# Kernel tuning notes

Measured on AMD Instinct MI355X. Metric: run time of the kernel, lower is better.

Reference implementation:

```python
import jax, jax.numpy as jnp
import numpy as np

B, S, D = 2, 2048, 2048
NH, NKV = 16, 4
HD = D // NH          # 128
Q_DIM = NH * HD       # 2048
KV_DIM = NKV * HD     # 512
N_REP = NH // NKV     # 4


def setup_inputs() -> dict:
    key = jax.random.key(0)
    k1, k2, k3, k4 = jax.random.split(key, 4)
    x = jax.random.normal(k1, (B, S, D), dtype=jnp.float32)
    freqs_cis = jax.random.normal(k2, (S, HD), dtype=jnp.float32)
    Wqkv = jax.random.normal(k3, (Q_DIM + 2 * KV_DIM, D), dtype=jnp.float32) * (D ** -0.5)
    Wo = jax.random.normal(k4, (D, Q_DIM), dtype=jnp.float32) * (Q_DIM ** -0.5)
    return {"x": x, "freqs_cis": freqs_cis, "Wqkv": Wqkv, "Wo": Wo}


def _apply_rope(xq, xk, freqs_cis):
    # xq: [B,S,NH,HD], xk: [B,S,NKV,HD], freqs_cis: [S,HD] viewed as [S,1,HD//2,2]
    f = freqs_cis.reshape(S, 1, HD // 2, 2)
    f0, f1 = f[..., 0], f[..., 1]  # broadcast over batch & heads

    def rot(t):
        shp = t.shape
        tp = t.reshape(*shp[:-1], HD // 2, 2)
        t0, t1 = tp[..., 0], tp[..., 1]
        # row1 = <x, (f0,f1)>;  row0 = <x, (f1,-f0)>  (matches torch flip+negate)
        row1 = t0 * f0 + t1 * f1
        row0 = t0 * f1 - t1 * f0
        return jnp.stack([row0, row1], axis=-1).reshape(shp)

    return rot(xq), rot(xk)


def reference(x, freqs_cis, Wqkv, Wo):
    # Fused QKV projection (exact path: all RLA sketch dims = 0)
    xqkv = jnp.einsum('bsd,od->bso', x, Wqkv)
    xq = xqkv[..., :Q_DIM].reshape(B, S, NH, HD)
    xk = xqkv[..., Q_DIM:Q_DIM + KV_DIM].reshape(B, S, NKV, HD)
    xv = xqkv[..., Q_DIM + KV_DIM:].reshape(B, S, NKV, HD)

    xq, xk = _apply_rope(xq, xk, freqs_cis)

    # [B,H,S,HD]
    xq = xq.transpose(0, 2, 1, 3)
    xk = xk.transpose(0, 2, 1, 3)
    xv = xv.transpose(0, 2, 1, 3)

    # GQA: repeat kv heads n_rep times
    xk = jnp.repeat(xk, N_REP, axis=1)
    xv = jnp.repeat(xv, N_REP, axis=1)

    scale = 1.0 / jnp.sqrt(jnp.asarray(HD, dtype=xq.dtype))
    scores = jnp.einsum('bhqd,bhkd->bhqk', xq, xk) * scale
    causal = jnp.tril(jnp.ones((S, S), dtype=bool))
    scores = jnp.where(causal, scores, jnp.finfo(scores.dtype).min)
    probs = jax.nn.softmax(scores, axis=-1)
    out = jnp.einsum('bhqk,bhkd->bhqd', probs, xv)  # [B,H,S,HD]

    out = out.transpose(0, 2, 1, 3).reshape(B, S, Q_DIM)
    return jnp.einsum('bsq,dq->bsd', out, Wo)
```

## Files before the change

### kernel.cpp

```cpp
#include <hip/hip_runtime.h>
#include <hip/hip_bf16.h>
#include <cstdint>
#include <cstddef>

#define B_ 2
#define S_ 2048
#define NH_ 16
#define NKV_ 4
#define HD_ 128
#define QDIM_ 2048
#define KVDIM_ 512
#define QKV_ 3072

typedef __attribute__((ext_vector_type(8))) short short8;
typedef __attribute__((ext_vector_type(4))) short bhalf4;
typedef __attribute__((ext_vector_type(4))) float float4v;

__device__ __forceinline__ float bf2f(short u) {
  union { unsigned int i; float f; } v;
  v.i = ((unsigned int)(unsigned short)u) << 16;
  return v.f;
}
__device__ __forceinline__ short f2bf(float f) {
  union { float f; unsigned int i; } v; v.f = f;
  unsigned int x = v.i;
  x += 0x7fffu + ((x >> 16) & 1u);
  return (short)(x >> 16);
}

__device__ __forceinline__ void async_copy16(void* lds, const void* g) {
  __builtin_amdgcn_global_load_lds(
      (const __attribute__((address_space(1))) void*)g,
      (__attribute__((address_space(3))) void*)lds, 16, 0, 0);
}

__global__ void f32_to_bf16(const float* __restrict__ src, short* __restrict__ dst,
                            int n8) {
  int id = blockIdx.x * 256 + threadIdx.x;
  if (id >= n8) return;
  const float* f = src + (size_t)id * 8;
  float4v a = *(const float4v*)(f);
  float4v b = *(const float4v*)(f + 4);
  short8 r;
#pragma unroll
  for (int e = 0; e < 4; ++e) { r[e] = f2bf(a[e]); r[4 + e] = f2bf(b[e]); }
  *(short8*)(dst + (size_t)id * 8) = r;
}

template <int N, int K, bool CF32>
__global__ __launch_bounds__(256)
void gemm_nt_bf16(const short* __restrict__ A, const short* __restrict__ Bm,
                  void* __restrict__ Cp) {
  __shared__ __align__(16) short sA[128 * 32];
  __shared__ __align__(16) short sB[128 * 32];
  const int tid = threadIdx.x;
  const int m0 = blockIdx.y * 128, n0 = blockIdx.x * 128;
  const int wave = tid >> 6, lane = tid & 63;
  const int wm = (wave & 1) << 6, wn = (wave >> 1) << 6;
  const int lm = lane & 15, kg = lane >> 4;

  float4v acc[4][4];
#pragma unroll
  for (int i = 0; i < 4; ++i)
#pragma unroll
    for (int j = 0; j < 4; ++j)
      acc[i][j] = (float4v){0.f, 0.f, 0.f, 0.f};

  const int r0 = tid >> 2, c0 = tid & 3;
  const short* gA0 = A + (size_t)(m0 + r0) * K + c0 * 8;
  const short* gA1 = gA0 + (size_t)64 * K;
  const short* gB0 = Bm + (size_t)(n0 + r0) * K + c0 * 8;
  const short* gB1 = gB0 + (size_t)64 * K;
  short* lA0 = sA + tid * 8;
  short* lA1 = sA + 2048 + tid * 8;
  short* lB0 = sB + tid * 8;
  short* lB1 = sB + 2048 + tid * 8;

  for (int k0 = 0; k0 < K; k0 += 32) {
    async_copy16(lA0, gA0 + k0);
    async_copy16(lA1, gA1 + k0);
    async_copy16(lB0, gB0 + k0);
    async_copy16(lB1, gB1 + k0);
    __syncthreads();

    short8 a[4], b[4];
#pragma unroll
    for (int i = 0; i < 4; ++i)
      a[i] = *(const short8*)(sA + (wm + i * 16 + lm) * 32 + kg * 8);
#pragma unroll
    for (int j = 0; j < 4; ++j)
      b[j] = *(const short8*)(sB + (wn + j * 16 + lm) * 32 + kg * 8);
#pragma unroll
    for (int i = 0; i < 4; ++i)
#pragma unroll
      for (int j = 0; j < 4; ++j)
        acc[i][j] = __builtin_amdgcn_mfma_f32_16x16x32_bf16(a[i], b[j], acc[i][j], 0, 0, 0);
    __syncthreads();
  }

#pragma unroll
  for (int i = 0; i < 4; ++i) {
    const int rb = m0 + wm + i * 16 + kg * 4;
#pragma unroll
    for (int j = 0; j < 4; ++j) {
      const int cc = n0 + wn + j * 16 + lm;
#pragma unroll
      for (int r = 0; r < 4; ++r) {
        if constexpr (CF32)
          ((float*)Cp)[(size_t)(rb + r) * N + cc] = acc[i][j][r];
        else
          ((short*)Cp)[(size_t)(rb + r) * N + cc] = f2bf(acc[i][j][r]);
      }
    }
  }
}

__global__ void rope_split(const short* __restrict__ xqkv, const float* __restrict__ freqs,
                           short* __restrict__ Qr, short* __restrict__ Kr,
                           short* __restrict__ Vv) {
  const int id = blockIdx.x * 256 + threadIdx.x;
  const int i = id / (QKV_ / 8);
  const int c8 = id % (QKV_ / 8);
  const int col = c8 * 8;
  const int b = i >> 11, s = i & (S_ - 1);
  short8 xv = *(const short8*)(xqkv + (size_t)i * QKV_ + col);
  if (col < QDIM_ + KVDIM_) {
    int d;
    short* dst;
    float sc;
    if (col < QDIM_) {
      int hh = col >> 7; d = col & 127;
      dst = Qr + ((size_t)(b * NH_ + hh) * S_ + s) * HD_ + d;
      sc = 0.08838834764831845f;
    } else {
      int cc = col - QDIM_;
      int hh = cc >> 7; d = cc & 127;
      dst = Kr + ((size_t)(b * NKV_ + hh) * S_ + s) * HD_ + d;
      sc = 1.0f;
    }
    const float* fp = freqs + (size_t)s * HD_ + d;
    float4v fa = *(const float4v*)(fp);
    float4v fb = *(const float4v*)(fp + 4);
    float ff[8] = {fa[0], fa[1], fa[2], fa[3], fb[0], fb[1], fb[2], fb[3]};
    short8 ov;
#pragma unroll
    for (int pp = 0; pp < 4; ++pp) {
      float t0 = bf2f(xv[2 * pp]), t1 = bf2f(xv[2 * pp + 1]);
      float f0 = ff[2 * pp], f1 = ff[2 * pp + 1];
      ov[2 * pp]     = f2bf((t0 * f1 - t1 * f0) * sc);
      ov[2 * pp + 1] = f2bf((t0 * f0 + t1 * f1) * sc);
    }
    *(short8*)dst = ov;
  } else {
    int cc = col - QDIM_ - KVDIM_;
    int hh = cc >> 7, d = cc & 127;
    *(short8*)(Vv + ((size_t)(b * NKV_ + hh) * S_ + s) * HD_ + d) = xv;
  }
}

__global__ void transpose_v(const short* __restrict__ Vv, short* __restrict__ Vt) {
  __shared__ short t[64][72];
  const int s0 = blockIdx.x * 64, d0 = blockIdx.y * 64;
  const short* src = Vv + (size_t)blockIdx.z * S_ * HD_;
  short* dst = Vt + (size_t)blockIdx.z * S_ * HD_;
  const int tid = threadIdx.x;
#pragma unroll
  for (int c = 0; c < 2; ++c) {
    int ch = tid + 256 * c;
    int row = ch >> 3, kc = ch & 7;
    *(short8*)(&t[row][kc * 8]) =
        *(const short8*)(src + (size_t)(s0 + row) * HD_ + d0 + kc * 8);
  }
  __syncthreads();
#pragma unroll
  for (int c = 0; c < 2; ++c) {
    int ch = tid + 256 * c;
    int drow = ch >> 3, sc = ch & 7;
    short8 w;
#pragma unroll
    for (int j = 0; j < 8; ++j) w[j] = t[sc * 8 + j][drow];
    *(short8*)(dst + (size_t)(d0 + drow) * S_ + s0 + sc * 8) = w;
  }
}

#define TK 64

__global__ __launch_bounds__(256)
void attn_causal(const short* __restrict__ Q, const short* __restrict__ K,
                 const short* __restrict__ Vt, short* __restrict__ O) {
  const int pair = blockIdx.x;
  const int bh = blockIdx.y;
  const int b = bh >> 4, h = bh & 15;
  const int kvh = h >> 2;
  const int tid = threadIdx.x, wave = tid >> 6, lane = tid & 63;
  const int lm = lane & 15, kg = lane >> 4;

  __shared__ __align__(16) short sK[TK * HD_];
  __shared__ __align__(16) short sVt[HD_ * TK];
  __shared__ __align__(16) short sO[4 * 16 * 128];

  const short* Qb = Q + (size_t)(b * NH_ + h) * S_ * HD_;
  const short* Kb = K + (size_t)(b * NKV_ + kvh) * S_ * HD_;
  const short* Vtb = Vt + (size_t)(b * NKV_ + kvh) * S_ * HD_;

  for (int half = 0; half < 2; ++half) {
    const int qt = (half == 0) ? pair : 31 - pair;
    const int q0w = qt * 64 + wave * 16;
    const int qglob = q0w + lm;

    short8 qf[4];
#pragma unroll
    for (int kk = 0; kk < 4; ++kk)
      qf[kk] = *(const short8*)(Qb + (size_t)qglob * HD_ + kk * 32 + kg * 8);

    float mcur = -1e9f, lcur = 0.f;
    float4v o[8];
#pragma unroll
    for (int df = 0; df < 8; ++df) o[df] = (float4v){0.f, 0.f, 0.f, 0.f};

    const int ntiles = qt + 1;
    for (int j = 0; j < ntiles; ++j) {
      const int k0 = j * TK;
#pragma unroll
      for (int c = 0; c < 4; ++c) {
        int ch = tid + 256 * c;
        int row = ch >> 4, kc = ch & 15;
        async_copy16(sK + ch * 8,
                     Kb + (size_t)(k0 + row) * HD_ + (kc ^ (row & 7)) * 8);
      }
#pragma unroll
      for (int c = 0; c < 4; ++c) {
        int ch = tid + 256 * c;
        int row = ch >> 3, kc = ch & 7;
        async_copy16(sVt + ch * 8,
                     Vtb + (size_t)row * S_ + k0 + (kc ^ (row & 7)) * 8);
      }
      __syncthreads();

      float4v sfT[4];
#pragma unroll
      for (int mj = 0; mj < 4; ++mj) sfT[mj] = (float4v){0.f, 0.f, 0.f, 0.f};
#pragma unroll
      for (int kk = 0; kk < 4; ++kk) {
        int kd = kk * 4 + kg;
#pragma unroll
        for (int mj = 0; mj < 4; ++mj) {
          int row = mj * 16 + lm;
          short8 af = *(const short8*)(sK + row * HD_ + (kd ^ (row & 7)) * 8);
          sfT[mj] = __builtin_amdgcn_mfma_f32_16x16x32_bf16(af, qf[kk], sfT[mj], 0, 0, 0);
        }
      }

      if (j == qt) {
#pragma unroll
        for (int mj = 0; mj < 4; ++mj)
#pragma unroll
          for (int r = 0; r < 4; ++r) {
            int kcol = k0 + mj * 16 + kg * 4 + r;
            sfT[mj][r] = (kcol <= qglob) ? sfT[mj][r] : -3e38f;
          }
      }

      float mx = -3e38f;
#pragma unroll
      for (int mj = 0; mj < 4; ++mj)
#pragma unroll
        for (int r = 0; r < 4; ++r) mx = fmaxf(mx, sfT[mj][r]);
      mx = fmaxf(mx, __shfl_xor(mx, 16, 64));
      mx = fmaxf(mx, __shfl_xor(mx, 32, 64));
      float mnew = fmaxf(mcur, mx);
      float alpha = __expf(fminf(mcur - mnew, 0.f));
      float rs = 0.f;
      bhalf4 pb[4];
#pragma unroll
      for (int t = 0; t < 4; ++t)
#pragma unroll
        for (int r = 0; r < 4; ++r) {
          float e = __expf(fminf(sfT[t][r] - mnew, 0.f));
          rs += e;
          pb[t][r] = f2bf(e);
        }
      rs += __shfl_xor(rs, 16, 64);
      rs += __shfl_xor(rs, 32, 64);
      mcur = mnew;
      lcur = lcur * alpha + rs;
#pragma unroll
      for (int df = 0; df < 8; ++df)
#pragma unroll
        for (int r = 0; r < 4; ++r) o[df][r] *= alpha;

#pragma unroll
      for (int t = 0; t < 4; ++t) {
        int kc = t * 2 + (kg >> 1);
#pragma unroll
        for (int df = 0; df < 8; ++df) {
          int row = df * 16 + lm;
          bhalf4 va = *(const bhalf4*)(sVt + row * TK + (kc ^ (row & 7)) * 8 +
                                       (kg & 1) * 4);
          o[df] = __builtin_amdgcn_mfma_f32_16x16x16bf16_1k(va, pb[t], o[df], 0, 0, 0);
        }
      }
      __syncthreads();
    }

    float inv = 1.f / lcur;
    short* myO = sO + wave * 2048;
#pragma unroll
    for (int df = 0; df < 8; ++df) {
      unsigned int p0 = (unsigned short)f2bf(o[df][0] * inv) |
                        ((unsigned int)(unsigned short)f2bf(o[df][1] * inv) << 16);
      unsigned int p1 = (unsigned short)f2bf(o[df][2] * inv) |
                        ((unsigned int)(unsigned short)f2bf(o[df][3] * inv) << 16);
      int base = lm * 128 + df * 16 + kg * 4;
      *(unsigned int*)(myO + base) = p0;
      *(unsigned int*)(myO + base + 2) = p1;
    }
    int q = lane >> 2, dp = (lane & 3) * 32;
    const size_t rowoff = (size_t)(b * S_ + q0w + q) * QDIM_ + h * HD_ + dp;
#pragma unroll
    for (int e = 0; e < 4; ++e) {
      short8 w = *(const short8*)(myO + q * 128 + dp + e * 8);
      *(short8*)(O + rowoff + e * 8) = w;
    }
  }
}

extern "C" void kernel_launch(void* const* d_in, const int* in_sizes, int n_in,
                              void* d_out, int out_size, void* d_ws, size_t ws_size,
                              hipStream_t stream) {
  const float* x     = (const float*)d_in[0];
  const float* freqs = (const float*)d_in[1];
  const float* Wqkv  = (const float*)d_in[2];
  const float* Wo    = (const float*)d_in[3];
  float* out = (float*)d_out;

  short* ws     = (short*)d_ws;
  short* xb     = ws;
  short* Wob    = ws;
  short* Wqkvb  = ws + (size_t)4096 * 2048;
  short* xqkv   = Wqkvb + (size_t)QKV_ * 2048;
  short* attn   = xqkv;
  short* Qr     = xqkv + (size_t)4096 * QKV_;
  short* Kr     = Qr + (size_t)B_ * NH_ * S_ * HD_;
  short* Vv     = Kr + (size_t)B_ * NKV_ * S_ * HD_;
  short* Vtg    = Vv + (size_t)B_ * NKV_ * S_ * HD_;

  f32_to_bf16<<<(4096 * 2048 / 8) / 256, 256, 0, stream>>>(x, xb, 4096 * 2048 / 8);
  f32_to_bf16<<<(QKV_ * 2048 / 8) / 256, 256, 0, stream>>>(Wqkv, Wqkvb, QKV_ * 2048 / 8);
  gemm_nt_bf16<QKV_, 2048, false>
      <<<dim3(QKV_ / 128, 4096 / 128), 256, 0, stream>>>(xb, Wqkvb, xqkv);
  f32_to_bf16<<<(2048 * 2048 / 8) / 256, 256, 0, stream>>>(Wo, Wob, 2048 * 2048 / 8);
  rope_split<<<(B_ * S_ * QKV_ / 8) / 256, 256, 0, stream>>>(xqkv, freqs, Qr, Kr, Vv);
  transpose_v<<<dim3(S_ / 64, HD_ / 64, B_ * NKV_), 256, 0, stream>>>(Vv, Vtg);
  attn_causal<<<dim3(16, B_ * NH_), 256, 0, stream>>>(Qr, Kr, Vtg, attn);
  gemm_nt_bf16<2048, 2048, true>
      <<<dim3(2048 / 128, 4096 / 128), 256, 0, stream>>>(attn, Wob, out);
}
```

Before: 328.7 us.

## Double-buffer K/V tiles and fuse both causal halves into one pipelined loop

The attention kernel now keeps two LDS buffers for K and V^T and issues the async copy of the next tile before computing on the current one, so global loads overlap with MFMA work. The two query tiles each block handles are merged into a single 33-step loop, which keeps the prefetch running across the boundary between halves. The epilogue and Q reload happen mid-loop. It also drops the fminf clamps before the exponentials. LDS use roughly doubles, which may lower occupancy, and there is now one barrier per iteration instead of two.

```diff
diff --git a/kernel.cpp b/kernel.cpp
--- a/kernel.cpp
+++ b/kernel.cpp
@@ -195,114 +195,45 @@
   const int tid = threadIdx.x, wave = tid >> 6, lane = tid & 63;
   const int lm = lane & 15, kg = lane >> 4;
 
-  __shared__ __align__(16) short sK[TK * HD_];
-  __shared__ __align__(16) short sVt[HD_ * TK];
+  __shared__ __align__(16) short sK[2][TK * HD_];
+  __shared__ __align__(16) short sVt[2][HD_ * TK];
   __shared__ __align__(16) short sO[4 * 16 * 128];
 
   const short* Qb = Q + (size_t)(b * NH_ + h) * S_ * HD_;
   const short* Kb = K + (size_t)(b * NKV_ + kvh) * S_ * HD_;
   const short* Vtb = Vt + (size_t)(b * NKV_ + kvh) * S_ * HD_;
 
-  for (int half = 0; half < 2; ++half) {
-    const int qt = (half == 0) ? pair : 31 - pair;
-    const int q0w = qt * 64 + wave * 16;
-    const int qglob = q0w + lm;
-
-    short8 qf[4];
-#pragma unroll
-    for (int kk = 0; kk < 4; ++kk)
-      qf[kk] = *(const short8*)(Qb + (size_t)qglob * HD_ + kk * 32 + kg * 8);
-
-    float mcur = -1e9f, lcur = 0.f;
-    float4v o[8];
-#pragma unroll
-    for (int df = 0; df < 8; ++df) o[df] = (float4v){0.f, 0.f, 0.f, 0.f};
-
-    const int ntiles = qt + 1;
-    for (int j = 0; j < ntiles; ++j) {
-      const int k0 = j * TK;
-#pragma unroll
-      for (int c = 0; c < 4; ++c) {
-        int ch = tid + 256 * c;
-        int row = ch >> 4, kc = ch & 15;
-        async_copy16(sK + ch * 8,
-                     Kb + (size_t)(k0 + row) * HD_ + (kc ^ (row & 7)) * 8);
-      }
-#pragma unroll
-      for (int c = 0; c < 4; ++c) {
-        int ch = tid + 256 * c;
-        int row = ch >> 3, kc = ch & 7;
-        async_copy16(sVt + ch * 8,
-                     Vtb + (size_t)row * S_ + k0 + (kc ^ (row & 7)) * 8);
-      }
-      __syncthreads();
-
-      float4v sfT[4];
-#pragma unroll
-      for (int mj = 0; mj < 4; ++mj) sfT[mj] = (float4v){0.f, 0.f, 0.f, 0.f};
-#pragma unroll
-      for (int kk = 0; kk < 4; ++kk) {
-        int kd = kk * 4 + kg;
-#pragma unroll
-        for (int mj = 0; mj < 4; ++mj) {
-          int row = mj * 16 + lm;
-          short8 af = *(const short8*)(sK + row * HD_ + (kd ^ (row & 7)) * 8);
-          sfT[mj] = __builtin_amdgcn_mfma_f32_16x16x32_bf16(af, qf[kk], sfT[mj], 0, 0, 0);
-        }
-      }
-
-      if (j == qt) {
-#pragma unroll
-        for (int mj = 0; mj < 4; ++mj)
-#pragma unroll
-          for (int r = 0; r < 4; ++r) {
-            int kcol = k0 + mj * 16 + kg * 4 + r;
-            sfT[mj][r] = (kcol <= qglob) ? sfT[mj][r] : -3e38f;
-          }
-      }
-
-      float mx = -3e38f;
-#pragma unroll
-      for (int mj = 0; mj < 4; ++mj)
-#pragma unroll
-        for (int r = 0; r < 4; ++r) mx = fmaxf(mx, sfT[mj][r]);
-      mx = fmaxf(mx, __shfl_xor(mx, 16, 64));
-      mx = fmaxf(mx, __shfl_xor(mx, 32, 64));
-      float mnew = fmaxf(mcur, mx);
-      float alpha = __expf(fminf(mcur - mnew, 0.f));
-      float rs = 0.f;
-      bhalf4 pb[4];
-#pragma unroll
-      for (int t = 0; t < 4; ++t)
-#pragma unroll
-        for (int r = 0; r < 4; ++r) {
-          float e = __expf(fminf(sfT[t][r] - mnew, 0.f));
-          rs += e;
-          pb[t][r] = f2bf(e);
-        }
-      rs += __shfl_xor(rs, 16, 64);
-      rs += __shfl_xor(rs, 32, 64);
-      mcur = mnew;
-      lcur = lcur * alpha + rs;
-#pragma unroll
-      for (int df = 0; df < 8; ++df)
-#pragma unroll
-        for (int r = 0; r < 4; ++r) o[df][r] *= alpha;
-
-#pragma unroll
-      for (int t = 0; t < 4; ++t) {
-        int kc = t * 2 + (kg >> 1);
-#pragma unroll
-        for (int df = 0; df < 8; ++df) {
-          int row = df * 16 + lm;
-          bhalf4 va = *(const bhalf4*)(sVt + row * TK + (kc ^ (row & 7)) * 8 +
-                                       (kg & 1) * 4);
-          o[df] = __builtin_amdgcn_mfma_f32_16x16x16bf16_1k(va, pb[t], o[df], 0, 0, 0);
-        }
-      }
-      __syncthreads();
-    }
-
+  const int qt0 = pair, qt1 = 31 - pair;
+  const int n0 = qt0 + 1;
+
+  auto stage = [&](int k0, int bf) {
+#pragma unroll
+    for (int c = 0; c < 4; ++c) {
+      int ch = tid + 256 * c;
+      int row = ch >> 4, kc = ch & 15;
+      async_copy16(sK[bf] + ch * 8,
+                   Kb + (size_t)(k0 + row) * HD_ + (kc ^ (row & 7)) * 8);
+    }
+#pragma unroll
+    for (int c = 0; c < 4; ++c) {
+      int ch = tid + 256 * c;
+      int row = ch >> 3, kc = ch & 7;
+      async_copy16(sVt[bf] + ch * 8,
+                   Vtb + (size_t)row * S_ + k0 + (kc ^ (row & 7)) * 8);
+    }
+  };
+
+  int qglob = qt0 * 64 + wave * 16 + lm;
+  short8 qf[4];
+#pragma unroll
+  for (int kk = 0; kk < 4; ++kk)
+    qf[kk] = *(const short8*)(Qb + (size_t)qglob * HD_ + kk * 32 + kg * 8);
+  float mcur = -1e9f, lcur = 0.f;
+  float4v o[8];
+#pragma unroll
+  for (int df = 0; df < 8; ++df) o[df] = (float4v){0.f, 0.f, 0.f, 0.f};
+
+  auto epilogue = [&](int q0w) {
     float inv = 1.f / lcur;
     short* myO = sO + wave * 2048;
 #pragma unroll
@@ -322,7 +253,100 @@
       short8 w = *(const short8*)(myO + q * 128 + dp + e * 8);
       *(short8*)(O + rowoff + e * 8) = w;
     }
-  }
+  };
+
+  stage(0, 0);
+
+  for (int s = 0; s < 33; ++s) {
+    const int bf = s & 1;
+    const bool h1 = (s >= n0);
+    const int k0 = (h1 ? (s - n0) : s) * TK;
+    const bool diag = h1 ? (s == 32) : (s == qt0);
+
+    __syncthreads();
+    if (s + 1 < 33) {
+      int sn = s + 1;
+      int k0n = ((sn >= n0) ? (sn - n0) : sn) * TK;
+      stage(k0n, sn & 1);
+    }
+
+    float4v sfT[4];
+#pragma unroll
+    for (int mj = 0; mj < 4; ++mj) sfT[mj] = (float4v){0.f, 0.f, 0.f, 0.f};
+#pragma unroll
+    for (int kk = 0; kk < 4; ++kk) {
+      int kd = kk * 4 + kg;
+#pragma unroll
+      for (int mj = 0; mj < 4; ++mj) {
+        int row = mj * 16 + lm;
+        short8 af = *(const short8*)(sK[bf] + row * HD_ + (kd ^ (row & 7)) * 8);
+        sfT[mj] = __builtin_amdgcn_mfma_f32_16x16x32_bf16(af, qf[kk], sfT[mj], 0, 0, 0);
+      }
+    }
+
+    if (diag) {
+#pragma unroll
+      for (int mj = 0; mj < 4; ++mj)
+#pragma unroll
+        for (int r = 0; r < 4; ++r) {
+          int kcol = k0 + mj * 16 + kg * 4 + r;
+          sfT[mj][r] = (kcol <= qglob) ? sfT[mj][r] : -3e38f;
+        }
+    }
+
+    float mx = -3e38f;
+#pragma unroll
+    for (int mj = 0; mj < 4; ++mj)
+#pragma unroll
+      for (int r = 0; r < 4; ++r) mx = fmaxf(mx, sfT[mj][r]);
+    mx = fmaxf(mx, __shfl_xor(mx, 16, 64));
+    mx = fmaxf(mx, __shfl_xor(mx, 32, 64));
+    float mnew = fmaxf(mcur, mx);
+    float alpha = __expf(mcur - mnew);
+    float rs = 0.f;
+    bhalf4 pb[4];
+#pragma unroll
+    for (int t = 0; t < 4; ++t)
+#pragma unroll
+      for (int r = 0; r < 4; ++r) {
+        float e = __expf(sfT[t][r] - mnew);
+        rs += e;
+        pb[t][r] = f2bf(e);
+      }
+    rs += __shfl_xor(rs, 16, 64);
+    rs += __shfl_xor(rs, 32, 64);
+    mcur = mnew;
+    lcur = lcur * alpha + rs;
+#pragma unroll
+    for (int df = 0; df < 8; ++df)
+#pragma unroll
+      for (int r = 0; r < 4; ++r) o[df][r] *= alpha;
+
+#pragma unroll
+    for (int t = 0; t < 4; ++t) {
+      int kc = t * 2 + (kg >> 1);
+#pragma unroll
+      for (int df = 0; df < 8; ++df) {
+        int row = df * 16 + lm;
+        bhalf4 va = *(const bhalf4*)(sVt[bf] + row * TK + (kc ^ (row & 7)) * 8 +
+                                     (kg & 1) * 4);
+        o[df] = __builtin_amdgcn_mfma_f32_16x16x16bf16_1k(va, pb[t], o[df], 0, 0, 0);
+      }
+    }
+
+    if (s == n0 - 1) {
+      epilogue(qt0 * 64 + wave * 16);
+      qglob = qt1 * 64 + wave * 16 + lm;
+#pragma unroll
+      for (int kk = 0; kk < 4; ++kk)
+        qf[kk] = *(const short8*)(Qb + (size_t)qglob * HD_ + kk * 32 + kg * 8);
+      mcur = -1e9f; lcur = 0.f;
+#pragma unroll
+      for (int df = 0; df < 8; ++df) o[df] = (float4v){0.f, 0.f, 0.f, 0.f};
+    }
+  }
+
+  epilogue(qt1 * 64 + wave * 16);
 }
 
 extern "C" void kernel_launch(void* const* d_in, const int* in_sizes, int n_in,
```

New measurement: 317.0 us. 3.6% less time.
